# Performance work log

Measured on AMD Instinct MI355X. Metric: run time of the kernel, lower is better.

Reference implementation:

```python
import jax, jax.numpy as jnp
import numpy as np

B, N, C, H = 2, 2048, 1024, 16
D = C // H  # head dim = 64


def setup_inputs() -> dict:
    key = jax.random.key(0)
    k1, k2, k3 = jax.random.split(key, 3)
    x = jax.random.normal(k1, (B, N, C), dtype=jnp.float32)
    w_qkv = jax.random.normal(k2, (C, 3 * C), dtype=jnp.float32) * 0.02
    w_proj = jax.random.normal(k3, (C, C), dtype=jnp.float32) * 0.02
    b_proj = jnp.zeros((C,), dtype=jnp.float32)
    return {"x": x, "w_qkv": w_qkv, "w_proj": w_proj, "b_proj": b_proj}


def reference(x, w_qkv, w_proj, b_proj):
    Bx, Nx, Cx = x.shape
    h, d = H, Cx // H
    # fused QKV projection (no bias: qkv_bias=False)
    qkv = x @ w_qkv  # [B, N, 3C]
    qkv = qkv.reshape(Bx, Nx, 3, h, d).transpose(2, 0, 3, 1, 4)  # [3, B, H, N, D]
    q, k, v = qkv[0], qkv[1], qkv[2]
    # scaled dot-product attention weights (full NxN matrix, as in flax)
    scale = jnp.asarray(1.0 / np.sqrt(d), dtype=x.dtype)
    scores = jnp.einsum('bhqd,bhkd->bhqk', q * scale, k)  # [B, H, N, N]
    attn = jax.nn.softmax(scores, axis=-1)
    # attention-value matmul, merge heads
    out = jnp.einsum('bhqk,bhkd->bhqd', attn, v)  # [B, H, N, D]
    out = out.swapaxes(1, 2).reshape(Bx, Nx, Cx)  # [B, N, C]
    # output projection (with bias: use_bias=True)
    return out @ w_proj + b_proj
```

## Files before the change

### kernel.cpp

```cpp
#include <hip/hip_runtime.h>
#include <cstdint>
#include <cstddef>

#define B_ 2
#define N_ 2048
#define C_ 1024
#define H_ 16

typedef unsigned short u16;
typedef __attribute__((ext_vector_type(8))) short bf16x8;
typedef __attribute__((ext_vector_type(4))) float f32x4;
typedef __attribute__((ext_vector_type(8))) u16 u16x8;
typedef __attribute__((ext_vector_type(4))) u16 u16x4;

static __device__ __forceinline__ u16 f2bf(float f) {
  unsigned int u = __builtin_bit_cast(unsigned int, f);
  u += 0x7FFFu + ((u >> 16) & 1u);
  return (u16)(u >> 16);
}

__global__ void cvt_f32_bf16(const float* __restrict__ in, u16* __restrict__ out) {
  const size_t i = (size_t)(blockIdx.x * blockDim.x + threadIdx.x) * 4;
  const float4 v = *(const float4*)(in + i);
  u16x4 o;
  o[0] = f2bf(v.x); o[1] = f2bf(v.y); o[2] = f2bf(v.z); o[3] = f2bf(v.w);
  *(u16x4*)(out + i) = o;
}

__global__ void tcvt_bf16(const float* __restrict__ in, u16* __restrict__ out,
                          int R, int Cn) {
  __shared__ float T[32][33];
  const int t = threadIdx.x;
  const int c0 = blockIdx.x * 32, r0 = blockIdx.y * 32;
  {
    const int r = t >> 3, c4 = (t & 7) * 4;
    const float4 v = *(const float4*)(in + (size_t)(r0 + r) * Cn + c0 + c4);
    T[r][c4 + 0] = v.x; T[r][c4 + 1] = v.y; T[r][c4 + 2] = v.z; T[r][c4 + 3] = v.w;
  }
  __syncthreads();
  {
    const int c = t >> 3, r4 = (t & 7) * 4;
    u16x4 o;
    o[0] = f2bf(T[r4 + 0][c]); o[1] = f2bf(T[r4 + 1][c]);
    o[2] = f2bf(T[r4 + 2][c]); o[3] = f2bf(T[r4 + 3][c]);
    *(u16x4*)(out + (size_t)(c0 + c) * R + r0 + r4) = o;
  }
}

__global__ __launch_bounds__(256, 4)
void vtrans(const u16* __restrict__ qkv, u16* __restrict__ vt) {
  __shared__ u16 T[64][72];
  const int tid = threadIdx.x;
  const int bh = blockIdx.x, tile = blockIdx.y;
  const int b = bh >> 4, h = bh & 15;
  const size_t src = (size_t)(b * N_ + tile * 64) * 3072 + 2048 + h * 64;
#pragma unroll
  for (int i = 0; i < 2; ++i) {
    const int f = tid + i * 256;
    const int row = f >> 3, d8 = (f & 7) * 8;
    *(u16x8*)&T[row][d8] = *(const u16x8*)(qkv + src + (size_t)row * 3072 + d8);
  }
  __syncthreads();
#pragma unroll
  for (int i = 0; i < 2; ++i) {
    const int f = tid + i * 256;
    const int d = f >> 3, n8 = (f & 7) * 8;
    u16x8 o;
#pragma unroll
    for (int j = 0; j < 8; ++j) o[j] = T[n8 + j][d];
    *(u16x8*)(vt + (size_t)(bh * 64 + d) * N_ + tile * 64 + n8) = o;
  }
}

template<bool BIAS, bool OUTBF>
__global__ __launch_bounds__(256, 2)
void gemm_bf16(const u16* __restrict__ A, const u16* __restrict__ Bt,
               const float* __restrict__ bias, float* __restrict__ Cf,
               u16* __restrict__ Cb, int M, int Nn, int K)
{
  __shared__ u16 As[128][40];
  __shared__ u16 Bs[128][40];

  const int tid = threadIdx.x;
  const int lane = tid & 63, wv = tid >> 6;
  const int wr = wv >> 1, wc = wv & 1;
  const int lr = lane & 15, lk = (lane >> 4) * 8;

  f32x4 acc[4][4];
#pragma unroll
  for (int m = 0; m < 4; ++m)
#pragma unroll
    for (int n = 0; n < 4; ++n) acc[m][n] = (f32x4){0.f, 0.f, 0.f, 0.f};

  const u16* Ag = A + (size_t)(blockIdx.y * 128) * K;
  const u16* Bg = Bt + (size_t)(blockIdx.x * 128) * K;

  for (int kt = 0; kt < K; kt += 32) {
#pragma unroll
    for (int i = 0; i < 2; ++i) {
      const int f = tid + i * 256;
      const int row = f >> 2, kq = (f & 3) * 8;
      *(u16x8*)&As[row][kq] = *(const u16x8*)(Ag + (size_t)row * K + kt + kq);
      *(u16x8*)&Bs[row][kq] = *(const u16x8*)(Bg + (size_t)row * K + kt + kq);
    }
    __syncthreads();

    bf16x8 a[4], b[4];
#pragma unroll
    for (int m = 0; m < 4; ++m) a[m] = *(bf16x8*)&As[wr * 64 + m * 16 + lr][lk];
#pragma unroll
    for (int n = 0; n < 4; ++n) b[n] = *(bf16x8*)&Bs[wc * 64 + n * 16 + lr][lk];
#pragma unroll
    for (int m = 0; m < 4; ++m)
#pragma unroll
      for (int n = 0; n < 4; ++n)
        acc[m][n] = __builtin_amdgcn_mfma_f32_16x16x32_bf16(a[m], b[n], acc[m][n], 0, 0, 0);
    __syncthreads();
  }

#pragma unroll
  for (int n = 0; n < 4; ++n) {
    const int col = blockIdx.x * 128 + wc * 64 + n * 16 + lr;
    const float bv = BIAS ? bias[col] : 0.f;
#pragma unroll
    for (int m = 0; m < 4; ++m) {
      const int rbase = blockIdx.y * 128 + wr * 64 + m * 16 + (lane >> 4) * 4;
#pragma unroll
      for (int r = 0; r < 4; ++r) {
        if (OUTBF) Cb[(size_t)(rbase + r) * Nn + col] = f2bf(acc[m][n][r]);
        else       Cf[(size_t)(rbase + r) * Nn + col] = acc[m][n][r] + bv;
      }
    }
  }
}

__global__ __launch_bounds__(256, 3)
void attn_mfma(const u16* __restrict__ qkv, const u16* __restrict__ vt,
               u16* __restrict__ att)
{
  __shared__ u16 Ks[2][64][72];
  __shared__ u16 Vs[2][64][72];
  __shared__ u16 Ps[64][72];

  const int tid = threadIdx.x;
  const int lane = tid & 63, wv = tid >> 6;
  const int l15 = lane & 15, lg = lane >> 4;
  const int bid = blockIdx.x;
  const int swz = (bid & 7) * 128 + (bid >> 3);
  const int bh = swz >> 5, qt = swz & 31;
  const int b = bh >> 4, h = bh & 15;

  const size_t qbase = (size_t)(b * N_ + qt * 64) * 3072 + h * 64;
  const size_t kcol  = (size_t)b * N_ * 3072 + 1024 + h * 64;
  const size_t vbase = (size_t)(bh * 64) * N_;

  const int f0 = tid, f1 = tid + 256;
  const int row0 = f0 >> 3, c80 = (f0 & 7) * 8;
  const int row1 = f1 >> 3, c81 = (f1 & 7) * 8;

  *(u16x8*)&Ps[row0][c80] = *(const u16x8*)(qkv + qbase + (size_t)row0 * 3072 + c80);
  *(u16x8*)&Ps[row1][c81] = *(const u16x8*)(qkv + qbase + (size_t)row1 * 3072 + c81);
  *(u16x8*)&Ks[0][row0][c80] = *(const u16x8*)(qkv + kcol + (size_t)row0 * 3072 + c80);
  *(u16x8*)&Ks[0][row1][c81] = *(const u16x8*)(qkv + kcol + (size_t)row1 * 3072 + c81);
  *(u16x8*)&Vs[0][row0][c80] = *(const u16x8*)(vt + vbase + (size_t)row0 * N_ + c80);
  *(u16x8*)&Vs[0][row1][c81] = *(const u16x8*)(vt + vbase + (size_t)row1 * N_ + c81);
  __syncthreads();
  bf16x8 qf[2];
#pragma unroll
  for (int ks = 0; ks < 2; ++ks) qf[ks] = *(bf16x8*)&Ps[wv * 16 + l15][ks * 32 + lg * 8];
  __syncthreads();

  f32x4 accO[4];
#pragma unroll
  for (int n = 0; n < 4; ++n) accO[n] = (f32x4){0.f, 0.f, 0.f, 0.f};
  float m[4] = {-INFINITY, -INFINITY, -INFINITY, -INFINITY};
  float l[4] = {0.f, 0.f, 0.f, 0.f};

  for (int t = 0; t < N_ / 64; ++t) {
    const int cur = t & 1;

    u16x8 k0, k1, v0, v1;
    if (t + 1 < N_ / 64) {
      const size_t krow = kcol + (size_t)((t + 1) * 64) * 3072;
      k0 = *(const u16x8*)(qkv + krow + (size_t)row0 * 3072 + c80);
      k1 = *(const u16x8*)(qkv + krow + (size_t)row1 * 3072 + c81);
      v0 = *(const u16x8*)(vt + vbase + (size_t)row0 * N_ + (t + 1) * 64 + c80);
      v1 = *(const u16x8*)(vt + vbase + (size_t)row1 * N_ + (t + 1) * 64 + c81);
    }

    f32x4 s[4];
#pragma unroll
    for (int n = 0; n < 4; ++n) {
      s[n] = (f32x4){0.f, 0.f, 0.f, 0.f};
#pragma unroll
      for (int ks = 0; ks < 2; ++ks) {
        const bf16x8 kf = *(bf16x8*)&Ks[cur][n * 16 + l15][ks * 32 + lg * 8];
        s[n] = __builtin_amdgcn_mfma_f32_16x16x32_bf16(qf[ks], kf, s[n], 0, 0, 0);
      }
    }

    float mx[4], scf[4], ps[4];
#pragma unroll
    for (int n = 0; n < 4; ++n)
#pragma unroll
      for (int r = 0; r < 4; ++r) s[n][r] *= 0.125f;
#pragma unroll
    for (int r = 0; r < 4; ++r)
      mx[r] = fmaxf(fmaxf(s[0][r], s[1][r]), fmaxf(s[2][r], s[3][r]));
#pragma unroll
    for (int mask = 1; mask < 16; mask <<= 1)
#pragma unroll
      for (int r = 0; r < 4; ++r) mx[r] = fmaxf(mx[r], __shfl_xor(mx[r], mask));
#pragma unroll
    for (int r = 0; r < 4; ++r) {
      const float mn = fmaxf(m[r], mx[r]);
      scf[r] = __expf(m[r] - mn);
      m[r] = mn;
      ps[r] = 0.f;
    }
#pragma unroll
    for (int n = 0; n < 4; ++n)
#pragma unroll
      for (int r = 0; r < 4; ++r) {
        const float p = __expf(s[n][r] - m[r]);
        s[n][r] = p;
        ps[r] += p;
      }
#pragma unroll
    for (int mask = 1; mask < 16; mask <<= 1)
#pragma unroll
      for (int r = 0; r < 4; ++r) ps[r] += __shfl_xor(ps[r], mask);
#pragma unroll
    for (int r = 0; r < 4; ++r) l[r] = l[r] * scf[r] + ps[r];
#pragma unroll
    for (int n = 0; n < 4; ++n)
#pragma unroll
      for (int r = 0; r < 4; ++r) accO[n][r] *= scf[r];

#pragma unroll
    for (int n = 0; n < 4; ++n)
#pragma unroll
      for (int r = 0; r < 4; ++r)
        Ps[wv * 16 + lg * 4 + r][n * 16 + l15] = f2bf(s[n][r]);

#pragma unroll
    for (int ks = 0; ks < 2; ++ks) {
      const bf16x8 pa = *(bf16x8*)&Ps[wv * 16 + l15][ks * 32 + lg * 8];
#pragma unroll
      for (int n = 0; n < 4; ++n) {
        const bf16x8 vf = *(bf16x8*)&Vs[cur][n * 16 + l15][ks * 32 + lg * 8];
        accO[n] = __builtin_amdgcn_mfma_f32_16x16x32_bf16(pa, vf, accO[n], 0, 0, 0);
      }
    }

    if (t + 1 < N_ / 64) {
      *(u16x8*)&Ks[cur ^ 1][row0][c80] = k0;
      *(u16x8*)&Ks[cur ^ 1][row1][c81] = k1;
      *(u16x8*)&Vs[cur ^ 1][row0][c80] = v0;
      *(u16x8*)&Vs[cur ^ 1][row1][c81] = v1;
    }
    __syncthreads();
  }

  float inv[4];
#pragma unroll
  for (int r = 0; r < 4; ++r) inv[r] = 1.f / l[r];
#pragma unroll
  for (int n = 0; n < 4; ++n) {
    const int col = h * 64 + n * 16 + l15;
#pragma unroll
    for (int r = 0; r < 4; ++r) {
      const int row = b * N_ + qt * 64 + wv * 16 + lg * 4 + r;
      att[(size_t)row * C_ + col] = f2bf(accO[n][r] * inv[r]);
    }
  }
}

extern "C" void kernel_launch(void* const* d_in, const int* in_sizes, int n_in,
                              void* d_out, int out_size, void* d_ws, size_t ws_size,
                              hipStream_t stream) {
  const float* x      = (const float*)d_in[0];
  const float* w_qkv  = (const float*)d_in[1];
  const float* w_proj = (const float*)d_in[2];
  const float* b_proj = (const float*)d_in[3];
  float* out = (float*)d_out;

  u16* qkvb = (u16*)d_ws;
  u16* xb   = qkvb + (size_t)4096 * 3072;
  u16* wqt  = xb   + (size_t)4096 * 1024;
  u16* wpt  = wqt  + (size_t)3072 * 1024;
  u16* aob  = wpt  + (size_t)1024 * 1024;
  u16* vt   = xb;

  const int M = B_ * N_;

  cvt_f32_bf16<<<4096, 256, 0, stream>>>(x, xb);
  tcvt_bf16<<<dim3(96, 32), 256, 0, stream>>>(w_qkv, wqt, C_, 3 * C_);
  tcvt_bf16<<<dim3(32, 32), 256, 0, stream>>>(w_proj, wpt, C_, C_);

  gemm_bf16<false, true><<<dim3(3 * C_ / 128, M / 128), 256, 0, stream>>>(
      xb, wqt, nullptr, nullptr, qkvb, M, 3 * C_, C_);

  vtrans<<<dim3(32, 32), 256, 0, stream>>>(qkvb, vt);

  attn_mfma<<<dim3(N_ / 64 * B_ * H_), 256, 0, stream>>>(qkvb, vt, aob);

  gemm_bf16<true, false><<<dim3(C_ / 128, M / 128), 256, 0, stream>>>(
      aob, wpt, b_proj, out, nullptr, M, C_, C_);
}
```

Baseline: 271.0 us.

## Fold log2e-scaled Q into QKV GEMM, enlarge attention tiles, add lazy rescale

The QKV GEMM epilogue now multiplies the Q columns by scale·log2(e), so the attention kernel can drop its per-score multiply and use exp2f. The attention block grows to 512 threads covering 128 query rows, so each K/V tile loaded into LDS serves twice as many queries and each thread prefetches one vector instead of two. Rescaling of the running max is skipped when every lane's new max stays within 11 of the old one. s_setprio is raised around the MFMA sections. The lazy rescale trades exact max tracking for fewer exp and multiply operations, and relies on fp32 headroom to keep values in range.

```diff
diff --git a/kernel.cpp b/kernel.cpp
--- a/kernel.cpp
+++ b/kernel.cpp
@@ -6,6 +6,7 @@
 #define N_ 2048
 #define C_ 1024
 #define H_ 16
+#define QSCALE 0.18033688f
 
 typedef unsigned short u16;
 typedef __attribute__((ext_vector_type(8))) short bf16x8;
@@ -76,7 +77,7 @@
 __global__ __launch_bounds__(256, 2)
 void gemm_bf16(const u16* __restrict__ A, const u16* __restrict__ Bt,
                const float* __restrict__ bias, float* __restrict__ Cf,
-               u16* __restrict__ Cb, int M, int Nn, int K)
+               u16* __restrict__ Cb, int M, int Nn, int K, float qscale)
 {
   __shared__ u16 As[128][40];
   __shared__ u16 Bs[128][40];
@@ -122,48 +123,45 @@
   for (int n = 0; n < 4; ++n) {
     const int col = blockIdx.x * 128 + wc * 64 + n * 16 + lr;
     const float bv = BIAS ? bias[col] : 0.f;
+    const float sc = (OUTBF && col < 1024) ? qscale : 1.0f;
 #pragma unroll
     for (int m = 0; m < 4; ++m) {
       const int rbase = blockIdx.y * 128 + wr * 64 + m * 16 + (lane >> 4) * 4;
 #pragma unroll
       for (int r = 0; r < 4; ++r) {
-        if (OUTBF) Cb[(size_t)(rbase + r) * Nn + col] = f2bf(acc[m][n][r]);
+        if (OUTBF) Cb[(size_t)(rbase + r) * Nn + col] = f2bf(acc[m][n][r] * sc);
         else       Cf[(size_t)(rbase + r) * Nn + col] = acc[m][n][r] + bv;
       }
     }
   }
 }
 
-__global__ __launch_bounds__(256, 3)
+__global__ __launch_bounds__(512, 2)
 void attn_mfma(const u16* __restrict__ qkv, const u16* __restrict__ vt,
                u16* __restrict__ att)
 {
   __shared__ u16 Ks[2][64][72];
   __shared__ u16 Vs[2][64][72];
-  __shared__ u16 Ps[64][72];
+  __shared__ u16 Ps[128][72];
 
   const int tid = threadIdx.x;
   const int lane = tid & 63, wv = tid >> 6;
   const int l15 = lane & 15, lg = lane >> 4;
   const int bid = blockIdx.x;
-  const int swz = (bid & 7) * 128 + (bid >> 3);
-  const int bh = swz >> 5, qt = swz & 31;
+  const int swz = (bid & 7) * 64 + (bid >> 3);
+  const int bh = swz >> 4, qt = swz & 15;
   const int b = bh >> 4, h = bh & 15;
 
-  const size_t qbase = (size_t)(b * N_ + qt * 64) * 3072 + h * 64;
+  const size_t qbase = (size_t)(b * N_ + qt * 128) * 3072 + h * 64;
   const size_t kcol  = (size_t)b * N_ * 3072 + 1024 + h * 64;
   const size_t vbase = (size_t)(bh * 64) * N_;
 
-  const int f0 = tid, f1 = tid + 256;
-  const int row0 = f0 >> 3, c80 = (f0 & 7) * 8;
-  const int row1 = f1 >> 3, c81 = (f1 & 7) * 8;
-
-  *(u16x8*)&Ps[row0][c80] = *(const u16x8*)(qkv + qbase + (size_t)row0 * 3072 + c80);
-  *(u16x8*)&Ps[row1][c81] = *(const u16x8*)(qkv + qbase + (size_t)row1 * 3072 + c81);
-  *(u16x8*)&Ks[0][row0][c80] = *(const u16x8*)(qkv + kcol + (size_t)row0 * 3072 + c80);
-  *(u16x8*)&Ks[0][row1][c81] = *(const u16x8*)(qkv + kcol + (size_t)row1 * 3072 + c81);
-  *(u16x8*)&Vs[0][row0][c80] = *(const u16x8*)(vt + vbase + (size_t)row0 * N_ + c80);
-  *(u16x8*)&Vs[0][row1][c81] = *(const u16x8*)(vt + vbase + (size_t)row1 * N_ + c81);
+  const int srow = tid >> 3, sc8 = (tid & 7) * 8;
+
+  *(u16x8*)&Ps[srow][sc8]      = *(const u16x8*)(qkv + qbase + (size_t)srow * 3072 + sc8);
+  *(u16x8*)&Ps[64 + srow][sc8] = *(const u16x8*)(qkv + qbase + (size_t)(64 + srow) * 3072 + sc8);
+  *(u16x8*)&Ks[0][srow][sc8]   = *(const u16x8*)(qkv + kcol + (size_t)srow * 3072 + sc8);
+  *(u16x8*)&Vs[0][srow][sc8]   = *(const u16x8*)(vt + vbase + (size_t)srow * N_ + sc8);
   __syncthreads();
   bf16x8 qf[2];
 #pragma unroll
@@ -179,16 +177,14 @@
   for (int t = 0; t < N_ / 64; ++t) {
     const int cur = t & 1;
 
-    u16x8 k0, k1, v0, v1;
+    u16x8 kpre, vpre;
     if (t + 1 < N_ / 64) {
-      const size_t krow = kcol + (size_t)((t + 1) * 64) * 3072;
-      k0 = *(const u16x8*)(qkv + krow + (size_t)row0 * 3072 + c80);
-      k1 = *(const u16x8*)(qkv + krow + (size_t)row1 * 3072 + c81);
-      v0 = *(const u16x8*)(vt + vbase + (size_t)row0 * N_ + (t + 1) * 64 + c80);
-      v1 = *(const u16x8*)(vt + vbase + (size_t)row1 * N_ + (t + 1) * 64 + c81);
+      kpre = *(const u16x8*)(qkv + kcol + (size_t)((t + 1) * 64 + srow) * 3072 + sc8);
+      vpre = *(const u16x8*)(vt + vbase + (size_t)srow * N_ + (t + 1) * 64 + sc8);
     }
 
     f32x4 s[4];
+    __builtin_amdgcn_s_setprio(1);
 #pragma unroll
     for (int n = 0; n < 4; ++n) {
       s[n] = (f32x4){0.f, 0.f, 0.f, 0.f};
@@ -198,12 +194,9 @@
         s[n] = __builtin_amdgcn_mfma_f32_16x16x32_bf16(qf[ks], kf, s[n], 0, 0, 0);
       }
     }
-
-    float mx[4], scf[4], ps[4];
-#pragma unroll
-    for (int n = 0; n < 4; ++n)
-#pragma unroll
-      for (int r = 0; r < 4; ++r) s[n][r] *= 0.125f;
+    __builtin_amdgcn_s_setprio(0);
+
+    float mx[4];
 #pragma unroll
     for (int r = 0; r < 4; ++r)
       mx[r] = fmaxf(fmaxf(s[0][r], s[1][r]), fmaxf(s[2][r], s[3][r]));
@@ -211,18 +204,27 @@
     for (int mask = 1; mask < 16; mask <<= 1)
 #pragma unroll
       for (int r = 0; r < 4; ++r) mx[r] = fmaxf(mx[r], __shfl_xor(mx[r], mask));
-#pragma unroll
-    for (int r = 0; r < 4; ++r) {
-      const float mn = fmaxf(m[r], mx[r]);
-      scf[r] = __expf(m[r] - mn);
-      m[r] = mn;
-      ps[r] = 0.f;
-    }
+
+    bool ok = true;
+#pragma unroll
+    for (int r = 0; r < 4; ++r) ok = ok && (mx[r] <= m[r] + 11.0f);
+    const bool skip = __all(ok);
+
+    float scf[4];
+    if (!skip) {
+#pragma unroll
+      for (int r = 0; r < 4; ++r) {
+        const float mn = fmaxf(m[r], mx[r]);
+        scf[r] = exp2f(m[r] - mn);
+        m[r] = mn;
+      }
+    }
+    float ps[4] = {0.f, 0.f, 0.f, 0.f};
 #pragma unroll
     for (int n = 0; n < 4; ++n)
 #pragma unroll
       for (int r = 0; r < 4; ++r) {
-        const float p = __expf(s[n][r] - m[r]);
+        const float p = exp2f(s[n][r] - m[r]);
         s[n][r] = p;
         ps[r] += p;
       }
@@ -230,12 +232,17 @@
     for (int mask = 1; mask < 16; mask <<= 1)
 #pragma unroll
       for (int r = 0; r < 4; ++r) ps[r] += __shfl_xor(ps[r], mask);
-#pragma unroll
-    for (int r = 0; r < 4; ++r) l[r] = l[r] * scf[r] + ps[r];
-#pragma unroll
-    for (int n = 0; n < 4; ++n)
-#pragma unroll
-      for (int r = 0; r < 4; ++r) accO[n][r] *= scf[r];
+    if (skip) {
+#pragma unroll
+      for (int r = 0; r < 4; ++r) l[r] += ps[r];
+    } else {
+#pragma unroll
+      for (int r = 0; r < 4; ++r) l[r] = l[r] * scf[r] + ps[r];
+#pragma unroll
+      for (int n = 0; n < 4; ++n)
+#pragma unroll
+        for (int r = 0; r < 4; ++r) accO[n][r] *= scf[r];
+    }
 
 #pragma unroll
     for (int n = 0; n < 4; ++n)
@@ -243,6 +250,7 @@
       for (int r = 0; r < 4; ++r)
         Ps[wv * 16 + lg * 4 + r][n * 16 + l15] = f2bf(s[n][r]);
 
+    __builtin_amdgcn_s_setprio(1);
 #pragma unroll
     for (int ks = 0; ks < 2; ++ks) {
       const bf16x8 pa = *(bf16x8*)&Ps[wv * 16 + l15][ks * 32 + lg * 8];
@@ -252,12 +260,11 @@
         accO[n] = __builtin_amdgcn_mfma_f32_16x16x32_bf16(pa, vf, accO[n], 0, 0, 0);
       }
     }
+    __builtin_amdgcn_s_setprio(0);
 
     if (t + 1 < N_ / 64) {
-      *(u16x8*)&Ks[cur ^ 1][row0][c80] = k0;
-      *(u16x8*)&Ks[cur ^ 1][row1][c81] = k1;
-      *(u16x8*)&Vs[cur ^ 1][row0][c80] = v0;
-      *(u16x8*)&Vs[cur ^ 1][row1][c81] = v1;
+      *(u16x8*)&Ks[cur ^ 1][srow][sc8] = kpre;
+      *(u16x8*)&Vs[cur ^ 1][srow][sc8] = vpre;
     }
     __syncthreads();
   }
@@ -270,7 +277,7 @@
     const int col = h * 64 + n * 16 + l15;
 #pragma unroll
     for (int r = 0; r < 4; ++r) {
-      const int row = b * N_ + qt * 64 + wv * 16 + lg * 4 + r;
+      const int row = b * N_ + qt * 128 + wv * 16 + lg * 4 + r;
       att[(size_t)row * C_ + col] = f2bf(accO[n][r] * inv[r]);
     }
   }
@@ -299,12 +306,12 @@
   tcvt_bf16<<<dim3(32, 32), 256, 0, stream>>>(w_proj, wpt, C_, C_);
 
   gemm_bf16<false, true><<<dim3(3 * C_ / 128, M / 128), 256, 0, stream>>>(
-      xb, wqt, nullptr, nullptr, qkvb, M, 3 * C_, C_);
+      xb, wqt, nullptr, nullptr, qkvb, M, 3 * C_, C_, QSCALE);
 
   vtrans<<<dim3(32, 32), 256, 0, stream>>>(qkvb, vt);
 
-  attn_mfma<<<dim3(N_ / 64 * B_ * H_), 256, 0, stream>>>(qkvb, vt, aob);
+  attn_mfma<<<dim3(N_ / 128 * B_ * H_), 512, 0, stream>>>(qkvb, vt, aob);
 
   gemm_bf16<true, false><<<dim3(C_ / 128, M / 128), 256, 0, stream>>>(
-      aob, wpt, b_proj, out, nullptr, M, C_, C_);
-}
+      aob, wpt, b_proj, out, nullptr, M, C_, C_, 1.0f);
+}
```

Result: no change. 266.5 us (-1.6%).
